# Kernel tuning notes

Measured on AMD Instinct MI355X. Metric: run time of the kernel, lower is better.

The kernel has to match this reference:

```python
import jax, jax.numpy as jnp
import numpy as np

H = 128
N_USER, N_TXN, N_DEVICE = 200000, 400000, 100000
E = 600000


def setup_inputs() -> dict:
    key = jax.random.key(0)
    ks = jax.random.split(key, 16)
    s = 0.05
    return {
        "x_user": jax.random.normal(ks[0], (N_USER, H), jnp.float32),
        "x_txn": jax.random.normal(ks[1], (N_TXN, H), jnp.float32),
        "x_device": jax.random.normal(ks[2], (N_DEVICE, H), jnp.float32),
        "es0": jax.random.randint(ks[3], (E,), 0, N_TXN),
        "ed0": jax.random.randint(ks[4], (E,), 0, N_USER),
        "es1": jax.random.randint(ks[5], (E,), 0, N_DEVICE),
        "ed1": jax.random.randint(ks[6], (E,), 0, N_USER),
        "es2": jax.random.randint(ks[7], (E,), 0, N_USER),
        "ed2": jax.random.randint(ks[8], (E,), 0, N_USER),
        "Wl": jax.random.normal(ks[9], (3, H, H), jnp.float32) * s,
        "bl": jax.random.normal(ks[10], (3, H), jnp.float32) * s,
        "Wr": jax.random.normal(ks[11], (3, H, H), jnp.float32) * s,
        "W1": jax.random.normal(ks[12], (H, 3 * H), jnp.float32) * s,
        "b1": jax.random.normal(ks[13], (H,), jnp.float32) * s,
        "W2": jax.random.normal(ks[14], (H, H), jnp.float32) * s,
        "b2": jax.random.normal(ks[15], (H,), jnp.float32) * s,
    }


def _sage(x_src, x_dst, es, ed, wl, b, wr):
    # PyG SAGEConv (mean aggr): lin_l(mean of neighbor feats) + lin_r(x_dst)
    n_dst = x_dst.shape[0]
    msgs = x_src[es]                                   # [E, H] gather
    agg = jax.ops.segment_sum(msgs, ed, num_segments=n_dst)   # [N_dst, H]
    cnt = jax.ops.segment_sum(jnp.ones((es.shape[0],), x_src.dtype), ed,
                              num_segments=n_dst)
    mean = agg / jnp.maximum(cnt, 1.0)[:, None]
    return mean @ wl.T + b + x_dst @ wr.T


def reference(x_user, x_txn, x_device, es0, ed0, es1, ed1, es2, ed2,
              Wl, bl, Wr, W1, b1, W2, b2):
    o0 = _sage(x_txn, x_user, es0, ed0, Wl[0], bl[0], Wr[0])
    o1 = _sage(x_device, x_user, es1, ed1, Wl[1], bl[1], Wr[1])
    o2 = _sage(x_user, x_user, es2, ed2, Wl[2], bl[2], Wr[2])
    combined = jnp.concatenate([o0, o1, o2], axis=-1)  # [N_user, 3H]
    h = jax.nn.relu(combined @ W1.T + b1)
    return h @ W2.T + b2
```

## Files before the change

### kernel.cpp

```cpp
#include <hip/hip_runtime.h>

#define H 128

__global__ __launch_bounds__(128) void precompute_kernel(
    const float* __restrict__ Wl, const float* __restrict__ bl,
    const float* __restrict__ Wr, const float* __restrict__ W1,
    const float* __restrict__ b1, const float* __restrict__ W2,
    const float* __restrict__ b2,
    float* __restrict__ Am, float* __restrict__ W2T,
    float* __restrict__ cvec, float* __restrict__ b2f)
{
  int b = blockIdx.x;
  int j = threadIdx.x;
  if (b < 512) {
    int mat = b >> 7;
    int m   = b & 127;
    float s = 0.f;
    if (mat < 3) {
      int r = mat;
      for (int i = 0; i < H; i++)
        s += Wl[r*H*H + i*H + m] * W1[j*3*H + r*H + i];
    } else {
      for (int r = 0; r < 3; r++)
        for (int i = 0; i < H; i++)
          s += Wr[r*H*H + i*H + m] * W1[j*3*H + r*H + i];
    }
    Am[mat*H*H + m*H + j] = s;
  } else if (b == 512) {
    float s = b1[j];
    for (int r = 0; r < 3; r++)
      for (int i = 0; i < H; i++)
        s += bl[r*H + i] * W1[j*3*H + r*H + i];
    cvec[j] = s;
    b2f[j]  = b2[j];
  } else {
    int m = b - 513;
    W2T[m*H + j] = W2[j*H + m];
  }
}

__global__ __launch_bounds__(256) void k_hist3(
    const int* __restrict__ ed0, const int* __restrict__ ed1,
    const int* __restrict__ ed2, int* __restrict__ cntA,
    int NU, int E0, int E1, int E2)
{
  int r = blockIdx.y;
  const int* ed = (r == 0) ? ed0 : (r == 1) ? ed1 : ed2;
  int E = (r == 0) ? E0 : (r == 1) ? E1 : E2;
  int i = blockIdx.x * 256 + threadIdx.x;
  if (i < E) atomicAdd(&cntA[(size_t)r * NU + ed[i]], 1);
}

__global__ __launch_bounds__(256) void k_scan1(
    const int* __restrict__ degA, int* __restrict__ offA,
    int* __restrict__ bsumA, int n, int nb1)
{
  int r = blockIdx.y;
  const int* deg = degA + (size_t)r * n;
  int* off1 = offA + (size_t)r * (n + 1);
  int* bsum = bsumA + (size_t)r * nb1;
  __shared__ int tmp[256];
  int i = blockIdx.x * 256 + threadIdx.x;
  int v = (i < n) ? deg[i] : 0;
  tmp[threadIdx.x] = v;
  __syncthreads();
  for (int s = 1; s < 256; s <<= 1) {
    int t = (threadIdx.x >= (unsigned)s) ? tmp[threadIdx.x - s] : 0;
    __syncthreads();
    tmp[threadIdx.x] += t;
    __syncthreads();
  }
  if (i < n) off1[i + 1] = tmp[threadIdx.x];
  if (threadIdx.x == 255) bsum[blockIdx.x] = tmp[255];
}

__global__ __launch_bounds__(1024) void k_scan2(int* __restrict__ bsumA,
                                                int nb, int nb1)
{
  int* bsum = bsumA + (size_t)blockIdx.y * nb1;
  __shared__ int tmp[1024];
  __shared__ int carry;
  if (threadIdx.x == 0) carry = 0;
  __syncthreads();
  for (int base = 0; base < nb; base += 1024) {
    int i = base + threadIdx.x;
    int v = (i < nb) ? bsum[i] : 0;
    tmp[threadIdx.x] = v;
    __syncthreads();
    for (int s = 1; s < 1024; s <<= 1) {
      int t = (threadIdx.x >= (unsigned)s) ? tmp[threadIdx.x - s] : 0;
      __syncthreads();
      tmp[threadIdx.x] += t;
      __syncthreads();
    }
    if (i < nb) bsum[i] = carry + tmp[threadIdx.x] - v;
    __syncthreads();
    if (threadIdx.x == 0) carry += tmp[1023];
    __syncthreads();
  }
}

__global__ __launch_bounds__(256) void k_scan3c(
    int* __restrict__ offA, const int* __restrict__ bsumA,
    int* __restrict__ curA, int n, int nb1)
{
  int r = blockIdx.y;
  int* off = offA + (size_t)r * (n + 1);
  const int* bsum = bsumA + (size_t)r * nb1;
  int* cur = curA + (size_t)r * n;
  int i = blockIdx.x * 256 + threadIdx.x;
  if (i < n) {
    int d = cur[i];
    int o = off[i + 1] + bsum[blockIdx.x];
    off[i + 1] = o;
    cur[i] = o - d;
  }
  if (blockIdx.x == 0 && threadIdx.x == 0) off[0] = 0;
}

__global__ __launch_bounds__(256) void k_scatter3(
    const int* __restrict__ es0, const int* __restrict__ es1,
    const int* __restrict__ es2,
    const int* __restrict__ ed0, const int* __restrict__ ed1,
    const int* __restrict__ ed2,
    int* __restrict__ curA,
    int* __restrict__ nbr0, int* __restrict__ nbr1, int* __restrict__ nbr2,
    int NU, int E0, int E1, int E2)
{
  int r = blockIdx.y;
  const int* es = (r == 0) ? es0 : (r == 1) ? es1 : es2;
  const int* ed = (r == 0) ? ed0 : (r == 1) ? ed1 : ed2;
  int* nbr = (r == 0) ? nbr0 : (r == 1) ? nbr1 : nbr2;
  int* cur = curA + (size_t)r * NU;
  int E = (r == 0) ? E0 : (r == 1) ? E1 : E2;
  int i = blockIdx.x * 256 + threadIdx.x;
  if (i < E) {
    int d = ed[i];
    int pos = atomicAdd(&cur[d], 1);
    nbr[pos] = es[i];
  }
}

__device__ __forceinline__ void mm_accum(const float* __restrict__ W,
                                         float (*xs)[130], float* wb,
                                         float2* acc0, float2* acc1,
                                         int tid, int nA, int c)
{
  for (int mc = 0; mc < 4; mc++) {
    __syncthreads();
    {
      int m = tid >> 3;
      const float4* s4 = (const float4*)(W + (size_t)(mc * 32 + m) * H + c * 16);
      float4* dd = (float4*)(wb + c * 516 + m * 16);
      dd[0] = s4[0]; dd[1] = s4[1]; dd[2] = s4[2]; dd[3] = s4[3];
    }
    __syncthreads();
    const float* xr0 = &xs[nA][mc * 32];
    const float* xr1 = &xs[nA + 32][mc * 32];
    const float4* wq = (const float4*)(wb + c * 516);
#pragma unroll 4
    for (int m = 0; m < 32; m++) {
      float xm0 = xr0[m], xm1 = xr1[m];
      const float4* w4 = wq + m * 4;
#pragma unroll
      for (int q = 0; q < 4; q++) {
        float4 w = w4[q];
        acc0[2*q].x   += xm0 * w.x; acc0[2*q].y   += xm0 * w.y;
        acc0[2*q+1].x += xm0 * w.z; acc0[2*q+1].y += xm0 * w.w;
        acc1[2*q].x   += xm1 * w.x; acc1[2*q].y   += xm1 * w.y;
        acc1[2*q+1].x += xm1 * w.z; acc1[2*q+1].y += xm1 * w.w;
      }
    }
  }
}

__global__ __launch_bounds__(256, 3) void k_fused(
    const float* __restrict__ xu, const float* __restrict__ xt,
    const float* __restrict__ xd,
    const int* __restrict__ off0, const int* __restrict__ nbr0,
    const int* __restrict__ off1, const int* __restrict__ nbr1,
    const int* __restrict__ off2, const int* __restrict__ nbr2,
    const float* __restrict__ Am, const float* __restrict__ W2T,
    const float* __restrict__ cvec, const float* __restrict__ b2f,
    float* __restrict__ out, int NU)
{
  __shared__ float xs[64][130];
  __shared__ float wb[8 * 516];
  int tid = threadIdx.x;
  int c = tid & 7, j0 = c * 16, nA = tid >> 3;
  int node = tid >> 2, q = tid & 3;
  int g0 = blockIdx.x * 64;
  int g = g0 + node;

  float2 acc0[8], acc1[8];
#pragma unroll
  for (int qq = 0; qq < 8; qq++) {
    acc0[qq] = make_float2(cvec[j0 + 2*qq], cvec[j0 + 2*qq + 1]);
    acc1[qq] = acc0[qq];
  }

  for (int s = 0; s < 4; s++) {
    __syncthreads();
    float4 A[8];
#pragma unroll
    for (int i = 0; i < 8; i++) A[i] = make_float4(0.f, 0.f, 0.f, 0.f);

    if (g < NU) {
      if (s == 3) {
        const float4* src = (const float4*)(xu + (size_t)g * H) + q * 8;
#pragma unroll
        for (int i = 0; i < 8; i++) A[i] = src[i];
      } else {
        const float* xsrc = (s == 0) ? xt : (s == 1) ? xd : xu;
        const int* offp = (s == 0) ? off0 : (s == 1) ? off1 : off2;
        const int* nbrp = (s == 0) ? nbr0 : (s == 1) ? nbr1 : nbr2;
        int beg = offp[g], end = offp[g + 1];
        for (int e = beg; e < end; e++) {
          int srow = nbrp[e];
          const float4* src = (const float4*)(xsrc + (size_t)srow * H) + q * 8;
          float4 v[8];
#pragma unroll
          for (int i = 0; i < 8; i++) v[i] = src[i];
#pragma unroll
          for (int i = 0; i < 8; i++) {
            A[i].x += v[i].x; A[i].y += v[i].y;
            A[i].z += v[i].z; A[i].w += v[i].w;
          }
        }
        int d = end - beg;
        float inv = 1.f / (float)(d > 0 ? d : 1);
#pragma unroll
        for (int i = 0; i < 8; i++) {
          A[i].x *= inv; A[i].y *= inv; A[i].z *= inv; A[i].w *= inv;
        }
      }
    }
    float* xrow = &xs[node][q * 32];
#pragma unroll
    for (int i = 0; i < 8; i++) {
      ((float2*)xrow)[2*i]     = make_float2(A[i].x, A[i].y);
      ((float2*)xrow)[2*i + 1] = make_float2(A[i].z, A[i].w);
    }
    __syncthreads();
    mm_accum(Am + (size_t)s * H * H, xs, wb, acc0, acc1, tid, nA, c);
  }

  __syncthreads();
#pragma unroll
  for (int qq = 0; qq < 8; qq++) {
    float2 a = acc0[qq], b = acc1[qq];
    xs[nA][j0 + 2*qq]       = a.x > 0.f ? a.x : 0.f;
    xs[nA][j0 + 2*qq + 1]   = a.y > 0.f ? a.y : 0.f;
    xs[nA+32][j0 + 2*qq]     = b.x > 0.f ? b.x : 0.f;
    xs[nA+32][j0 + 2*qq + 1] = b.y > 0.f ? b.y : 0.f;
  }
  __syncthreads();
#pragma unroll
  for (int qq = 0; qq < 8; qq++) {
    acc0[qq] = make_float2(b2f[j0 + 2*qq], b2f[j0 + 2*qq + 1]);
    acc1[qq] = acc0[qq];
  }
  mm_accum(W2T, xs, wb, acc0, acc1, tid, nA, c);

  int gA = g0 + nA, gB = gA + 32;
  if (gA < NU) {
    float4* po = (float4*)(out + (size_t)gA * H + j0);
#pragma unroll
    for (int qq = 0; qq < 4; qq++)
      po[qq] = make_float4(acc0[2*qq].x, acc0[2*qq].y, acc0[2*qq+1].x, acc0[2*qq+1].y);
  }
  if (gB < NU) {
    float4* po = (float4*)(out + (size_t)gB * H + j0);
#pragma unroll
    for (int qq = 0; qq < 4; qq++)
      po[qq] = make_float4(acc1[2*qq].x, acc1[2*qq].y, acc1[2*qq+1].x, acc1[2*qq+1].y);
  }
}

extern "C" void kernel_launch(void* const* d_in, const int* in_sizes, int n_in,
                              void* d_out, int out_size, void* d_ws, size_t ws_size,
                              hipStream_t stream) {
  (void)n_in; (void)out_size; (void)ws_size;
  const float* xu = (const float*)d_in[0];
  const float* xt = (const float*)d_in[1];
  const float* xd = (const float*)d_in[2];
  const int* ess[3] = { (const int*)d_in[3], (const int*)d_in[5], (const int*)d_in[7] };
  const int* eds[3] = { (const int*)d_in[4], (const int*)d_in[6], (const int*)d_in[8] };
  const float* Wl = (const float*)d_in[9];
  const float* bl = (const float*)d_in[10];
  const float* Wr = (const float*)d_in[11];
  const float* W1 = (const float*)d_in[12];
  const float* b1 = (const float*)d_in[13];
  const float* W2 = (const float*)d_in[14];
  const float* b2 = (const float*)d_in[15];
  int Es[3] = { in_sizes[3], in_sizes[5], in_sizes[7] };
  int Emax = Es[0] > Es[1] ? Es[0] : Es[1];
  if (Es[2] > Emax) Emax = Es[2];

  const int NU = in_sizes[0] / H;
  const int NB = (NU + 255) / 256;
  float* out = (float*)d_out;

  char* p = (char*)d_ws;
  size_t pos = 0;
  auto take = [&](size_t bytes) -> char* {
    char* r = p + pos;
    pos = (pos + bytes + 255) & ~(size_t)255;
    return r;
  };
  float* Am   = (float*)take((size_t)4 * H * H * sizeof(float));
  float* W2T  = (float*)take((size_t)H * H * sizeof(float));
  float* cvec = (float*)take(512);
  float* b2f  = (float*)take(512);
  int* curA   = (int*)take((size_t)3 * NU * sizeof(int));
  int* offA   = (int*)take((size_t)3 * (NU + 1) * sizeof(int));
  int* bsumA  = (int*)take((size_t)3 * (NB + 1) * sizeof(int));
  int* nbr[3];
  for (int r = 0; r < 3; r++) nbr[r] = (int*)take((size_t)Es[r] * sizeof(int));

  precompute_kernel<<<641, 128, 0, stream>>>(Wl, bl, Wr, W1, b1, W2, b2,
                                             Am, W2T, cvec, b2f);
  hipMemsetAsync(curA, 0, (size_t)3 * NU * sizeof(int), stream);

  dim3 ge((Emax + 255) / 256, 3);
  dim3 gn(NB, 3);
  k_hist3<<<ge, 256, 0, stream>>>(eds[0], eds[1], eds[2], curA,
                                  NU, Es[0], Es[1], Es[2]);
  k_scan1<<<gn, 256, 0, stream>>>(curA, offA, bsumA, NU, NB + 1);
  k_scan2<<<dim3(1, 3), 1024, 0, stream>>>(bsumA, NB, NB + 1);
  k_scan3c<<<gn, 256, 0, stream>>>(offA, bsumA, curA, NU, NB + 1);
  k_scatter3<<<ge, 256, 0, stream>>>(ess[0], ess[1], ess[2],
                                     eds[0], eds[1], eds[2],
                                     curA, nbr[0], nbr[1], nbr[2],
                                     NU, Es[0], Es[1], Es[2]);

  k_fused<<<(NU + 63) / 64, 256, 0, stream>>>(
      xu, xt, xd,
      offA, nbr[0], offA + (NU + 1), nbr[1], offA + 2 * (NU + 1), nbr[2],
      Am, W2T, cvec, b2f, out, NU);
}
```

Baseline: 1.089 ms.

## Halve fused tile to 32 nodes, use packed FMA, fold scan2 into scan3

The fused SAGE+MLP kernel now handles 32 user nodes per block instead of 64. Each thread accumulates one node's 16 outputs, using 2-wide vector multiply-adds meant to map to packed FP32 FMA. The gather uses 8 threads per node instead of 4, and the occupancy hint rises from 3 to 4 blocks per CU. The separate single-block scan2 kernel is removed: each scan3c block now reduces all preceding block sums itself, trading a serial launch for redundant reads. Halving the tile means every block reloads the full weight matrices for half as many nodes, doubling weight staging traffic per node.

```diff
diff --git a/kernel.cpp b/kernel.cpp
--- a/kernel.cpp
+++ b/kernel.cpp
@@ -1,6 +1,8 @@
 #include <hip/hip_runtime.h>
 
 #define H 128
+
+typedef float v2f __attribute__((ext_vector_type(2)));
 
 __global__ __launch_bounds__(128) void precompute_kernel(
     const float* __restrict__ Wl, const float* __restrict__ bl,
@@ -74,32 +76,6 @@
   if (threadIdx.x == 255) bsum[blockIdx.x] = tmp[255];
 }
 
-__global__ __launch_bounds__(1024) void k_scan2(int* __restrict__ bsumA,
-                                                int nb, int nb1)
-{
-  int* bsum = bsumA + (size_t)blockIdx.y * nb1;
-  __shared__ int tmp[1024];
-  __shared__ int carry;
-  if (threadIdx.x == 0) carry = 0;
-  __syncthreads();
-  for (int base = 0; base < nb; base += 1024) {
-    int i = base + threadIdx.x;
-    int v = (i < nb) ? bsum[i] : 0;
-    tmp[threadIdx.x] = v;
-    __syncthreads();
-    for (int s = 1; s < 1024; s <<= 1) {
-      int t = (threadIdx.x >= (unsigned)s) ? tmp[threadIdx.x - s] : 0;
-      __syncthreads();
-      tmp[threadIdx.x] += t;
-      __syncthreads();
-    }
-    if (i < nb) bsum[i] = carry + tmp[threadIdx.x] - v;
-    __syncthreads();
-    if (threadIdx.x == 0) carry += tmp[1023];
-    __syncthreads();
-  }
-}
-
 __global__ __launch_bounds__(256) void k_scan3c(
     int* __restrict__ offA, const int* __restrict__ bsumA,
     int* __restrict__ curA, int n, int nb1)
@@ -108,10 +84,20 @@
   int* off = offA + (size_t)r * (n + 1);
   const int* bsum = bsumA + (size_t)r * nb1;
   int* cur = curA + (size_t)r * n;
+  __shared__ int red[256];
+  int a = 0;
+  for (int i = threadIdx.x; i < blockIdx.x; i += 256) a += bsum[i];
+  red[threadIdx.x] = a;
+  __syncthreads();
+  for (int s = 128; s > 0; s >>= 1) {
+    if (threadIdx.x < (unsigned)s) red[threadIdx.x] += red[threadIdx.x + s];
+    __syncthreads();
+  }
+  int prefix = red[0];
   int i = blockIdx.x * 256 + threadIdx.x;
   if (i < n) {
     int d = cur[i];
-    int o = off[i + 1] + bsum[blockIdx.x];
+    int o = off[i + 1] + prefix;
     off[i + 1] = o;
     cur[i] = o - d;
   }
@@ -143,8 +129,7 @@
 
 __device__ __forceinline__ void mm_accum(const float* __restrict__ W,
                                          float (*xs)[130], float* wb,
-                                         float2* acc0, float2* acc1,
-                                         int tid, int nA, int c)
+                                         v2f* acc, int tid, int nA, int c)
 {
   for (int mc = 0; mc < 4; mc++) {
     __syncthreads();
@@ -155,26 +140,26 @@
       dd[0] = s4[0]; dd[1] = s4[1]; dd[2] = s4[2]; dd[3] = s4[3];
     }
     __syncthreads();
-    const float* xr0 = &xs[nA][mc * 32];
-    const float* xr1 = &xs[nA + 32][mc * 32];
+    const float* xr = &xs[nA][mc * 32];
     const float4* wq = (const float4*)(wb + c * 516);
 #pragma unroll 4
     for (int m = 0; m < 32; m++) {
-      float xm0 = xr0[m], xm1 = xr1[m];
+      float xm = xr[m];
+      v2f xv; xv[0] = xm; xv[1] = xm;
       const float4* w4 = wq + m * 4;
 #pragma unroll
       for (int q = 0; q < 4; q++) {
         float4 w = w4[q];
-        acc0[2*q].x   += xm0 * w.x; acc0[2*q].y   += xm0 * w.y;
-        acc0[2*q+1].x += xm0 * w.z; acc0[2*q+1].y += xm0 * w.w;
-        acc1[2*q].x   += xm1 * w.x; acc1[2*q].y   += xm1 * w.y;
-        acc1[2*q+1].x += xm1 * w.z; acc1[2*q+1].y += xm1 * w.w;
+        v2f w01; w01[0] = w.x; w01[1] = w.y;
+        v2f w23; w23[0] = w.z; w23[1] = w.w;
+        acc[2*q]   += xv * w01;
+        acc[2*q+1] += xv * w23;
       }
     }
   }
 }
 
-__global__ __launch_bounds__(256, 3) void k_fused(
+__global__ __launch_bounds__(256, 4) void k_fused(
     const float* __restrict__ xu, const float* __restrict__ xt,
     const float* __restrict__ xd,
     const int* __restrict__ off0, const int* __restrict__ nbr0,
@@ -184,32 +169,32 @@
     const float* __restrict__ cvec, const float* __restrict__ b2f,
     float* __restrict__ out, int NU)
 {
-  __shared__ float xs[64][130];
+  __shared__ float xs[32][130];
   __shared__ float wb[8 * 516];
   int tid = threadIdx.x;
   int c = tid & 7, j0 = c * 16, nA = tid >> 3;
-  int node = tid >> 2, q = tid & 3;
-  int g0 = blockIdx.x * 64;
-  int g = g0 + node;
-
-  float2 acc0[8], acc1[8];
-#pragma unroll
-  for (int qq = 0; qq < 8; qq++) {
-    acc0[qq] = make_float2(cvec[j0 + 2*qq], cvec[j0 + 2*qq + 1]);
-    acc1[qq] = acc0[qq];
+  int q = tid & 7;
+  int g0 = blockIdx.x * 32;
+  int g = g0 + nA;
+
+  v2f acc[8];
+  {
+    const v2f* cv = (const v2f*)(cvec + j0);
+#pragma unroll
+    for (int qq = 0; qq < 8; qq++) acc[qq] = cv[qq];
   }
 
   for (int s = 0; s < 4; s++) {
     __syncthreads();
-    float4 A[8];
-#pragma unroll
-    for (int i = 0; i < 8; i++) A[i] = make_float4(0.f, 0.f, 0.f, 0.f);
+    float4 A[4];
+#pragma unroll
+    for (int i = 0; i < 4; i++) A[i] = make_float4(0.f, 0.f, 0.f, 0.f);
 
     if (g < NU) {
       if (s == 3) {
-        const float4* src = (const float4*)(xu + (size_t)g * H) + q * 8;
-#pragma unroll
-        for (int i = 0; i < 8; i++) A[i] = src[i];
+        const float4* src = (const float4*)(xu + (size_t)g * H) + q * 4;
+#pragma unroll
+        for (int i = 0; i < 4; i++) A[i] = src[i];
       } else {
         const float* xsrc = (s == 0) ? xt : (s == 1) ? xd : xu;
         const int* offp = (s == 0) ? off0 : (s == 1) ? off1 : off2;
@@ -217,12 +202,12 @@
         int beg = offp[g], end = offp[g + 1];
         for (int e = beg; e < end; e++) {
           int srow = nbrp[e];
-          const float4* src = (const float4*)(xsrc + (size_t)srow * H) + q * 8;
-          float4 v[8];
-#pragma unroll
-          for (int i = 0; i < 8; i++) v[i] = src[i];
-#pragma unroll
-          for (int i = 0; i < 8; i++) {
+          const float4* src = (const float4*)(xsrc + (size_t)srow * H) + q * 4;
+          float4 v[4];
+#pragma unroll
+          for (int i = 0; i < 4; i++) v[i] = src[i];
+#pragma unroll
+          for (int i = 0; i < 4; i++) {
             A[i].x += v[i].x; A[i].y += v[i].y;
             A[i].z += v[i].z; A[i].w += v[i].w;
           }
@@ -230,50 +215,46 @@
         int d = end - beg;
         float inv = 1.f / (float)(d > 0 ? d : 1);
 #pragma unroll
-        for (int i = 0; i < 8; i++) {
+        for (int i = 0; i < 4; i++) {
           A[i].x *= inv; A[i].y *= inv; A[i].z *= inv; A[i].w *= inv;
         }
       }
     }
-    float* xrow = &xs[node][q * 32];
-#pragma unroll
-    for (int i = 0; i < 8; i++) {
-      ((float2*)xrow)[2*i]     = make_float2(A[i].x, A[i].y);
-      ((float2*)xrow)[2*i + 1] = make_float2(A[i].z, A[i].w);
-    }
-    __syncthreads();
-    mm_accum(Am + (size_t)s * H * H, xs, wb, acc0, acc1, tid, nA, c);
+    {
+      float2* xrow = (float2*)&xs[nA][q * 16];
+#pragma unroll
+      for (int i = 0; i < 4; i++) {
+        xrow[2*i]     = make_float2(A[i].x, A[i].y);
+        xrow[2*i + 1] = make_float2(A[i].z, A[i].w);
+      }
+    }
+    __syncthreads();
+    mm_accum(Am + (size_t)s * H * H, xs, wb, acc, tid, nA, c);
   }
 
   __syncthreads();
-#pragma unroll
-  for (int qq = 0; qq < 8; qq++) {
-    float2 a = acc0[qq], b = acc1[qq];
-    xs[nA][j0 + 2*qq]       = a.x > 0.f ? a.x : 0.f;
-    xs[nA][j0 + 2*qq + 1]   = a.y > 0.f ? a.y : 0.f;
-    xs[nA+32][j0 + 2*qq]     = b.x > 0.f ? b.x : 0.f;
-    xs[nA+32][j0 + 2*qq + 1] = b.y > 0.f ? b.y : 0.f;
+  {
+    float2* xrow = (float2*)&xs[nA][j0];
+#pragma unroll
+    for (int qq = 0; qq < 8; qq++) {
+      float a0 = acc[qq][0], a1 = acc[qq][1];
+      xrow[qq] = make_float2(a0 > 0.f ? a0 : 0.f, a1 > 0.f ? a1 : 0.f);
+    }
   }
   __syncthreads();
-#pragma unroll
-  for (int qq = 0; qq < 8; qq++) {
-    acc0[qq] = make_float2(b2f[j0 + 2*qq], b2f[j0 + 2*qq + 1]);
-    acc1[qq] = acc0[qq];
-  }
-  mm_accum(W2T, xs, wb, acc0, acc1, tid, nA, c);
-
-  int gA = g0 + nA, gB = gA + 32;
-  if (gA < NU) {
-    float4* po = (float4*)(out + (size_t)gA * H + j0);
+  {
+    const v2f* bv = (const v2f*)(b2f + j0);
+#pragma unroll
+    for (int qq = 0; qq < 8; qq++) acc[qq] = bv[qq];
+  }
+  mm_accum(W2T, xs, wb, acc, tid, nA, c);
+
+  if (g < NU) {
+    float4* po = (float4*)(out + (size_t)g * H + j0);
 #pragma unroll
     for (int qq = 0; qq < 4; qq++)
-      po[qq] = make_float4(acc0[2*qq].x, acc0[2*qq].y, acc0[2*qq+1].x, acc0[2*qq+1].y);
-  }
-  if (gB < NU) {
-    float4* po = (float4*)(out + (size_t)gB * H + j0);
-#pragma unroll
-    for (int qq = 0; qq < 4; qq++)
-      po[qq] = make_float4(acc1[2*qq].x, acc1[2*qq].y, acc1[2*qq+1].x, acc1[2*qq+1].y);
+      po[qq] = make_float4(acc[2*qq][0], acc[2*qq][1],
+                           acc[2*qq+1][0], acc[2*qq+1][1]);
   }
 }
 
@@ -327,14 +308,13 @@
   k_hist3<<<ge, 256, 0, stream>>>(eds[0], eds[1], eds[2], curA,
                                   NU, Es[0], Es[1], Es[2]);
   k_scan1<<<gn, 256, 0, stream>>>(curA, offA, bsumA, NU, NB + 1);
-  k_scan2<<<dim3(1, 3), 1024, 0, stream>>>(bsumA, NB, NB + 1);
   k_scan3c<<<gn, 256, 0, stream>>>(offA, bsumA, curA, NU, NB + 1);
   k_scatter3<<<ge, 256, 0, stream>>>(ess[0], ess[1], ess[2],
                                      eds[0], eds[1], eds[2],
                                      curA, nbr[0], nbr[1], nbr[2],
                                      NU, Es[0], Es[1], Es[2]);
 
-  k_fused<<<(NU + 63) / 64, 256, 0, stream>>>(
+  k_fused<<<(NU + 31) / 32, 256, 0, stream>>>(
       xu, xt, xd,
       offA, nbr[0], offA + (NU + 1), nbr[1], offA + 2 * (NU + 1), nbr[2],
       Am, W2T, cvec, b2f, out, NU);
```

Result: slower. 1.205 ms (+10.7%).
